# Kernel optimization log

Measured on AMD Instinct MI355X. Metric: run time of the kernel, lower is better.

Reference implementation:

```python
import jax, jax.numpy as jnp
import numpy as np

DIM = 768
NUM_HEADS = 12
HEAD_DIM = DIM // NUM_HEADS
H, W = 16, 64
HK, WK = 7, 11
N = H * W
B = 8
SCALE = HEAD_DIM ** -0.5


def build_local_mask():
    # Vectorized version of the original nested loop: for each token (h,w),
    # positions inside the hk x wk window are visible (0), others -inf.
    h_idx = np.repeat(np.arange(H), W)  # [N]
    w_idx = np.tile(np.arange(W), H)    # [N]
    hh = np.arange(H + HK - 1)
    ww = np.arange(W + WK - 1)
    in_h = (hh[None, :] >= h_idx[:, None]) & (hh[None, :] < h_idx[:, None] + HK)  # [N, H+hk-1]
    in_w = (ww[None, :] >= w_idx[:, None]) & (ww[None, :] < w_idx[:, None] + WK)  # [N, W+wk-1]
    visible = in_h[:, :, None] & in_w[:, None, :]  # [N, H+hk-1, W+wk-1]
    mask_big = np.where(visible, 0.0, 1.0).astype(np.float32)
    mask_crop = mask_big[:, HK // 2:H + HK // 2, WK // 2:W + WK // 2].reshape(N, N)
    mask = np.where(mask_crop < 1.0, mask_crop, np.float32(-np.inf))  # [N, N]
    return jnp.asarray(mask)[None, None]  # [1, 1, N, N]


def setup_inputs() -> dict:
    key = jax.random.key(0)
    k1, k2, k3 = jax.random.split(key, 3)
    x = jax.random.normal(k1, (B, N, DIM), dtype=jnp.float32)
    w_qkv = jax.random.normal(k2, (3 * DIM, DIM), dtype=jnp.float32) * 0.02  # torch Linear weight [out,in]
    w_proj = jax.random.normal(k3, (DIM, DIM), dtype=jnp.float32) * 0.02
    b_proj = jnp.zeros((DIM,), dtype=jnp.float32)
    mask = build_local_mask()
    return {"x": x, "w_qkv": w_qkv, "w_proj": w_proj, "b_proj": b_proj, "mask": mask}


def reference(x, w_qkv, w_proj, b_proj, mask):
    Bx, Nx, C = x.shape
    qkv = jnp.einsum('bnc,oc->bno', x, w_qkv)  # [B, N, 3*dim]
    qkv = qkv.reshape(Bx, Nx, 3, NUM_HEADS, HEAD_DIM).transpose(2, 0, 3, 1, 4)  # [3,B,h,N,d]
    q, k, v = qkv[0] * SCALE, qkv[1], qkv[2]
    attn = jnp.einsum('bhnd,bhmd->bhnm', q, k) + mask  # [B,h,N,N] with local -inf mask
    attn = jax.nn.softmax(attn, axis=-1)
    out = jnp.einsum('bhnm,bhmd->bhnd', attn, v)  # [B,h,N,d]
    out = out.transpose(0, 2, 1, 3).reshape(Bx, Nx, C)
    out = jnp.einsum('bnc,oc->bno', out, w_proj) + b_proj
    return out
```

## Files before the change

### kernel.cpp

```cpp
#include <hip/hip_runtime.h>
#include <hip/hip_bf16.h>
#include <stdint.h>

typedef __bf16 bf16;
typedef __bf16 bf16x8 __attribute__((ext_vector_type(8)));
typedef __bf16 bf16x4 __attribute__((ext_vector_type(4)));
typedef float f32x4 __attribute__((ext_vector_type(4)));

#define KDIM 768
#define NHEAD 12
#define HDIM 64
#define NTOK 1024
#define BATCH 8

#define SWZ(row, b) ((b) ^ (((row) & 7) << 4))

__device__ __forceinline__ void gl_lds16(const bf16* g, bf16* l) {
    __builtin_amdgcn_global_load_lds((const __attribute__((address_space(1))) void*)g,
                                     (__attribute__((address_space(3))) void*)l, 16, 0, 0);
}

__global__ void k_cvt_all(const float* __restrict__ x, const float* __restrict__ wq,
                          const float* __restrict__ wp, bf16* __restrict__ xb,
                          bf16* __restrict__ wqb, bf16* __restrict__ wpb) {
    int b = blockIdx.x;
    const float* src;
    bf16* dst;
    int base;
    if (b < 6144)       { src = x;  dst = xb;  base = b; }
    else if (b < 7872)  { src = wq; dst = wqb; base = b - 6144; }
    else                { src = wp; dst = wpb; base = b - 7872; }
    int i = (base * 256 + threadIdx.x) * 4;
    float4 v = *(const float4*)(src + i);
    bf16x4 o;
    o[0] = (bf16)v.x; o[1] = (bf16)v.y; o[2] = (bf16)v.z; o[3] = (bf16)v.w;
    *(bf16x4*)(dst + i) = o;
}

#define BM 128
#define BN 128
#define BK 32

#define STAGE_G(Ab, Wb, Abuf, Bbuf, k0) do {                                   \
    gl_lds16((Ab) + (size_t)sr0 * KDIM + (k0) + sc0, (Abuf) + wv * 512);        \
    gl_lds16((Ab) + (size_t)sr1 * KDIM + (k0) + sc1, (Abuf) + 2048 + wv * 512); \
    gl_lds16((Wb) + (size_t)sr0 * KDIM + (k0) + sc0, (Bbuf) + wv * 512);        \
    gl_lds16((Wb) + (size_t)sr1 * KDIM + (k0) + sc1, (Bbuf) + 2048 + wv * 512); \
} while (0)

#define GEMM_PRE()                                                              \
    const int t = threadIdx.x;                                                  \
    const int lane = t & 63;                                                    \
    const int wv = t >> 6;                                                      \
    const int wr = wv >> 1, wc = wv & 1;                                        \
    const int lr = lane & 15, lg = lane >> 4;                                   \
             \
    const int q0 = wv * 64 + lane;                                              \
    const int R0 = q0 >> 3, wp0 = (q0 & 7) ^ (R0 & 7);                          \
    const int sr0 = 2 * R0 + (wp0 >> 2), sc0 = (wp0 & 3) * 8;                   \
    const int q1 = 256 + wv * 64 + lane;                                        \
    const int R1 = q1 >> 3, wp1 = (q1 & 7) ^ (R1 & 7);                          \
    const int sr1 = 2 * R1 + (wp1 >> 2), sc1 = (wp1 & 3) * 8;                   \
                                                         \
    const int rhalf = lr >> 1;                                                  \
    const int xorp = (((lr & 1) * 64 + lg * 16) ^ (rhalf << 4));

#define GEMM_LOOP(Ab, Wb)                                                       \
    f32x4 acc[4][4] = {};                                                       \
    STAGE_G(Ab, Wb, As[0], Bs[0], 0);                                           \
    STAGE_G(Ab, Wb, As[1], Bs[1], BK);                                          \
    asm volatile("s_waitcnt vmcnt(4)" ::: "memory");                            \
    __builtin_amdgcn_s_barrier();                                               \
    for (int tt = 0; tt < 24; ++tt) {                                           \
        int p = tt & 1;                                                         \
        const char* Ab8 = (const char*)As[p];                                   \
        const char* Bb8 = (const char*)Bs[p];                                   \
        bf16x8 af[4], bfr[4];                                                   \
        _Pragma("unroll")                                                       \
        for (int m = 0; m < 4; ++m)                                             \
            af[m] = *(const bf16x8*)(Ab8 + (wr * 32 + m * 8 + rhalf) * 128 + xorp); \
        _Pragma("unroll")                                                       \
        for (int n = 0; n < 4; ++n)                                             \
            bfr[n] = *(const bf16x8*)(Bb8 + (wc * 32 + n * 8 + rhalf) * 128 + xorp); \
        asm volatile("s_waitcnt lgkmcnt(0)" ::: "memory");                      \
        __builtin_amdgcn_s_barrier();                                           \
        if (tt < 22) {                                                          \
            STAGE_G(Ab, Wb, As[p], Bs[p], (tt + 2) * BK);                       \
            __builtin_amdgcn_sched_barrier(0);                                  \
        }                                                                       \
        _Pragma("unroll")                                                       \
        for (int m = 0; m < 4; ++m)                                             \
            _Pragma("unroll")                                                   \
            for (int n = 0; n < 4; ++n)                                         \
                acc[m][n] = __builtin_amdgcn_mfma_f32_16x16x32_bf16(af[m], bfr[n], acc[m][n], 0, 0, 0); \
        if (tt < 22)       { asm volatile("s_waitcnt vmcnt(4)" ::: "memory"); } \
        else if (tt == 22) { asm volatile("s_waitcnt vmcnt(0)" ::: "memory"); } \
        __builtin_amdgcn_s_barrier();                                           \
    }

__global__ __launch_bounds__(256) void k_gemm_qkv(
    const bf16* __restrict__ A, const bf16* __restrict__ W,
    bf16* __restrict__ qb, bf16* __restrict__ kb, bf16* __restrict__ vb)
{
    __shared__ bf16 As[2][BM * BK];
    __shared__ bf16 Bs[2][BN * BK];
    GEMM_PRE();
    const int bm = blockIdx.x, bn = blockIdx.y;
    const bf16* Ab = A + (size_t)bm * BM * KDIM;
    const bf16* Wb = W + (size_t)bn * BN * KDIM;
    GEMM_LOOP(Ab, Wb);

    const float QSC = 0.18033688011112042f;
#pragma unroll
    for (int n = 0; n < 4; ++n) {
        int o = bn * BN + wc * 64 + n * 16 + lr;
        int s = o / 768;
        int rem = o - s * 768;
        int head = rem >> 6;
        int d = o & 63;
        bf16* dst = (s == 0) ? qb : ((s == 1) ? kb : vb);
        float sc = (s == 0) ? QSC : 1.0f;
#pragma unroll
        for (int m = 0; m < 4; ++m) {
            int grow = bm * BM + wr * 64 + m * 16 + lg * 4;
            int bidx = grow >> 10;
            int tok = grow & 1023;
            size_t base = (((size_t)bidx * NHEAD + head) * NTOK + tok) * HDIM + d;
#pragma unroll
            for (int r = 0; r < 4; ++r)
                dst[base + (size_t)r * HDIM] = (bf16)(acc[m][n][r] * sc);
        }
    }
}

__global__ __launch_bounds__(256) void k_gemm_proj(
    const bf16* __restrict__ A, const bf16* __restrict__ W,
    const float* __restrict__ bias, float* __restrict__ out)
{
    __shared__ bf16 As[2][BM * BK];
    __shared__ bf16 Bs[2][BN * BK];
    GEMM_PRE();
    const int bm = blockIdx.x, bn = blockIdx.y;
    const bf16* Ab = A + (size_t)bm * BM * KDIM;
    const bf16* Wb = W + (size_t)bn * BN * KDIM;
    GEMM_LOOP(Ab, Wb);

#pragma unroll
    for (int n = 0; n < 4; ++n) {
        int col = bn * BN + wc * 64 + n * 16 + lr;
        float bv = bias[col];
#pragma unroll
        for (int m = 0; m < 4; ++m) {
            int grow = bm * BM + wr * 64 + m * 16 + lg * 4;
#pragma unroll
            for (int r = 0; r < 4; ++r)
                out[(size_t)(grow + r) * KDIM + col] = acc[m][n][r] + bv;
        }
    }
}

__global__ __launch_bounds__(256) void k_attn(
    const bf16* __restrict__ qbuf, const bf16* __restrict__ kbuf,
    const bf16* __restrict__ vbuf, bf16* __restrict__ ob)
{
    const int x = blockIdx.x;
    const int sub = x >> 3;
    const int bh = (x & 7) * 12 + (sub >> 4);
    const int qblk = sub & 15;
    const int head = bh % NHEAD, bidx = bh / NHEAD;
    const bf16* Q  = qbuf + (size_t)bh * NTOK * HDIM;
    const bf16* Kp = kbuf + (size_t)bh * NTOK * HDIM;
    const bf16* Vp = vbuf + (size_t)bh * NTOK * HDIM;

    const int t = threadIdx.x, lane = t & 63, wv = t >> 6;
    const int lr = lane & 15, lg = lane >> 4, lkb = lg * 8;

    __shared__ bf16 Ks[2][64 * 64];
    __shared__ bf16 vT[2][64 * 64];
    __shared__ bf16 pls[4][16 * 64];

    {
        bf16x8 z = {};
        *(bf16x8*)&pls[wv][lane * 16] = z;
        *(bf16x8*)&pls[wv][lane * 16 + 8] = z;
    }

    bf16x8 qf[2];
#pragma unroll
    for (int ks = 0; ks < 2; ++ks)
        qf[ks] = *(const bf16x8*)(Q + (size_t)(qblk * 64 + wv * 16 + lr) * HDIM + ks * 32 + lkb);

    f32x4 acc[4] = {};
    float mrow[4] = {-1e30f, -1e30f, -1e30f, -1e30f};
    float lrow[4] = {0.f, 0.f, 0.f, 0.f};

    const int kh0 = (qblk - 3 < 0) ? 0 : qblk - 3;
    const int kh1 = (qblk + 3 > 15) ? 15 : qblk + 3;

    const int sj = t >> 2;
    const int sd = (t & 3) * 16;

    const bf16* ks0 = Kp + (size_t)(kh0 * 64 + sj) * HDIM + sd;
    const bf16* vs0 = Vp + (size_t)(kh0 * 64 + sj) * HDIM + sd;
    bf16x8 gk0 = *(const bf16x8*)ks0, gk1 = *(const bf16x8*)(ks0 + 8);
    bf16x8 gv0 = *(const bf16x8*)vs0, gv1 = *(const bf16x8*)(vs0 + 8);

    char* pb8 = (char*)pls[wv];
    const int wq0 = wv * 16 + lg * 4;
    int cur = 0;

    for (int kh = kh0; kh <= kh1; ++kh) {
        char* kb8 = (char*)Ks[cur];
        char* vb8 = (char*)vT[cur];
        {
            int kbo = sj * 128 + sd * 2;
            *(bf16x8*)(kb8 + SWZ(sj, kbo)) = gk0;
            *(bf16x8*)(kb8 + SWZ(sj, kbo + 16)) = gk1;
        }
#pragma unroll
        for (int ii = 0; ii < 8; ++ii) {
            int d = sd + ii;
            *(bf16*)(vb8 + SWZ(d, (d << 7) + (sj << 1))) = gv0[ii];
        }
#pragma unroll
        for (int ii = 0; ii < 8; ++ii) {
            int d = sd + 8 + ii;
            *(bf16*)(vb8 + SWZ(d, (d << 7) + (sj << 1))) = gv1[ii];
        }
        if (kh < kh1) {
            const bf16* kn = Kp + (size_t)((kh + 1) * 64 + sj) * HDIM + sd;
            const bf16* vn = Vp + (size_t)((kh + 1) * 64 + sj) * HDIM + sd;
            gk0 = *(const bf16x8*)kn; gk1 = *(const bf16x8*)(kn + 8);
            gv0 = *(const bf16x8*)vn; gv1 = *(const bf16x8*)(vn + 8);
        }
        asm volatile("s_waitcnt lgkmcnt(0)" ::: "memory");
        __builtin_amdgcn_s_barrier();

        f32x4 s[3];
#pragma unroll
        for (int jj = 0; jj < 3; ++jj) {
            int j = wv - 1 + jj;
            if (j >= 0 && j <= 3) {
                int key = j * 16 + lr;
                int kbase = key * 128;
                bf16x8 kf0 = *(const bf16x8*)(kb8 + SWZ(key, kbase + lg * 16));
                bf16x8 kf1 = *(const bf16x8*)(kb8 + SWZ(key, kbase + 64 + lg * 16));
                f32x4 sv = {};
                sv = __builtin_amdgcn_mfma_f32_16x16x32_bf16(qf[0], kf0, sv, 0, 0, 0);
                sv = __builtin_amdgcn_mfma_f32_16x16x32_bf16(qf[1], kf1, sv, 0, 0, 0);
#pragma unroll
                for (int r = 0; r < 4; ++r) {
                    int dw = wq0 + r - key;
                    sv[r] = (dw >= -5 && dw <= 5) ? sv[r] : -1e30f;
                }
                s[jj] = sv;
            } else {
                s[jj] = f32x4{-1e30f, -1e30f, -1e30f, -1e30f};
            }
        }

        float pm[4], scl[4];
#pragma unroll
        for (int r = 0; r < 4; ++r) pm[r] = fmaxf(fmaxf(s[0][r], s[1][r]), s[2][r]);
#pragma unroll
        for (int off = 1; off < 16; off <<= 1)
#pragma unroll
            for (int r = 0; r < 4; ++r) pm[r] = fmaxf(pm[r], __shfl_xor(pm[r], off));
#pragma unroll
        for (int r = 0; r < 4; ++r) {
            float mn = fmaxf(mrow[r], pm[r]);
            scl[r] = exp2f(mrow[r] - mn);
            mrow[r] = mn;
        }
#pragma unroll
        for (int dt = 0; dt < 4; ++dt)
#pragma unroll
            for (int r = 0; r < 4; ++r) acc[dt][r] *= scl[r];

        float psum[4] = {0.f, 0.f, 0.f, 0.f};
#pragma unroll
        for (int jj = 0; jj < 3; ++jj) {
            int j = wv - 1 + jj;
            if (j >= 0 && j <= 3) {
#pragma unroll
                for (int r = 0; r < 4; ++r) {
                    float p = exp2f(s[jj][r] - mrow[r]);
                    psum[r] += p;
                    int row = lg * 4 + r;
                    *(bf16*)(pb8 + SWZ(row, row * 128 + (j * 16 + lr) * 2)) = (bf16)p;
                }
            }
        }
#pragma unroll
        for (int r = 0; r < 4; ++r) lrow[r] = lrow[r] * scl[r] + psum[r];

        bf16x8 pf0 = *(const bf16x8*)(pb8 + SWZ(lr, lr * 128 + lg * 16));
        bf16x8 pf1 = *(const bf16x8*)(pb8 + SWZ(lr, lr * 128 + 64 + lg * 16));
#pragma unroll
        for (int dt = 0; dt < 4; ++dt) {
            int vrow = dt * 16 + lr;
            bf16x8 vf0 = *(const bf16x8*)(vb8 + SWZ(vrow, vrow * 128 + lg * 16));
            bf16x8 vf1 = *(const bf16x8*)(vb8 + SWZ(vrow, vrow * 128 + 64 + lg * 16));
            acc[dt] = __builtin_amdgcn_mfma_f32_16x16x32_bf16(pf0, vf0, acc[dt], 0, 0, 0);
            acc[dt] = __builtin_amdgcn_mfma_f32_16x16x32_bf16(pf1, vf1, acc[dt], 0, 0, 0);
        }
        cur ^= 1;
    }

#pragma unroll
    for (int off = 1; off < 16; off <<= 1)
#pragma unroll
        for (int r = 0; r < 4; ++r) lrow[r] += __shfl_xor(lrow[r], off);

#pragma unroll
    for (int r = 0; r < 4; ++r) {
        float inv = 1.0f / lrow[r];
        int tok = qblk * 64 + wv * 16 + lg * 4 + r;
        size_t rowbase = ((size_t)bidx * NTOK + tok) * KDIM + head * HDIM;
#pragma unroll
        for (int dt = 0; dt < 4; ++dt)
            ob[rowbase + dt * 16 + lr] = (bf16)(acc[dt][r] * inv);
    }
}

extern "C" void kernel_launch(void* const* d_in, const int* in_sizes, int n_in,
                              void* d_out, int out_size, void* d_ws, size_t ws_size,
                              hipStream_t stream) {
    const float* x      = (const float*)d_in[0];
    const float* w_qkv  = (const float*)d_in[1];
    const float* w_proj = (const float*)d_in[2];
    const float* b_proj = (const float*)d_in[3];
    float* out = (float*)d_out;

    char* ws = (char*)d_ws;
    bf16* xb  = (bf16*)(ws);
    bf16* wqb = (bf16*)(ws + 12582912);
    bf16* wpb = (bf16*)(ws + 16121856);
    bf16* qb  = (bf16*)(ws + 17301504);
    bf16* kb  = (bf16*)(ws + 29884416);
    bf16* vb  = (bf16*)(ws + 42467328);
    bf16* aob = (bf16*)(ws + 55050240);

    hipLaunchKernelGGL(k_cvt_all, dim3(8448), dim3(256), 0, stream, x, w_qkv, w_proj, xb, wqb, wpb);
    hipLaunchKernelGGL(k_gemm_qkv, dim3(64, 18), dim3(256), 0, stream, xb, wqb, qb, kb, vb);
    hipLaunchKernelGGL(k_attn,     dim3(1536), dim3(256), 0, stream, qb, kb, vb, aob);
    hipLaunchKernelGGL(k_gemm_proj, dim3(64, 6), dim3(256), 0, stream, aob, wpb, b_proj, out);
}
```

Baseline: 105.6 us.

## Rework GEMMs to 128x256 tiles with 8 waves and triple-buffered BK=64 pipeline

Replaces the 128x128, BK=32 double-buffered GEMM with a 128x256 tile computed by 512 threads (2x4 waves), a BK=64 K-step and a three-stage LDS ring. Global-to-LDS loads are split across two halves of each iteration and interleaved with MFMA groups, and setprio is raised around the MFMAs. The intent is more reuse per loaded byte, fewer barriers per FLOP and better overlap of loads with compute. In exchange it uses much more LDS (144 KB per block), which limits occupancy, and it launches fewer blocks (576 for QKV, 192 for the projection), which may underfill the GPU.

```diff
diff --git a/kernel.cpp b/kernel.cpp
--- a/kernel.cpp
+++ b/kernel.cpp
@@ -37,83 +37,120 @@
     *(bf16x4*)(dst + i) = o;
 }
 
-#define BM 128
-#define BN 128
-#define BK 32
-
-#define STAGE_G(Ab, Wb, Abuf, Bbuf, k0) do {                                   \
-    gl_lds16((Ab) + (size_t)sr0 * KDIM + (k0) + sc0, (Abuf) + wv * 512);        \
-    gl_lds16((Ab) + (size_t)sr1 * KDIM + (k0) + sc1, (Abuf) + 2048 + wv * 512); \
-    gl_lds16((Wb) + (size_t)sr0 * KDIM + (k0) + sc0, (Bbuf) + wv * 512);        \
-    gl_lds16((Wb) + (size_t)sr1 * KDIM + (k0) + sc1, (Bbuf) + 2048 + wv * 512); \
+
+#define G_MFMA(a, b, c) __builtin_amdgcn_mfma_f32_16x16x32_bf16(a, b, c, 0, 0, 0)
+
+#define LOADA(SC)                                                              \
+    _Pragma("unroll")                                                          \
+    for (int m = 0; m < 4; ++m) {                                              \
+        const char* rp = (const char*)sA[SC] + (wr * 64 + m * 16 + lr) * 128;  \
+        af[m][0] = *(const bf16x8*)(rp + k0off);                               \
+        af[m][1] = *(const bf16x8*)(rp + k1off);                               \
+    }
+
+#define LOADB(SC, n0, bfr)                                                     \
+    _Pragma("unroll")                                                          \
+    for (int nn = 0; nn < 2; ++nn) {                                           \
+        const char* rp = (const char*)sB[SC] + (wc * 64 + ((n0) + nn) * 16 + lr) * 128; \
+        bfr[nn][0] = *(const bf16x8*)(rp + k0off);                             \
+        bfr[nn][1] = *(const bf16x8*)(rp + k1off);                             \
+    }
+
+#define MMQ(ch, bfr)                                                           \
+    __builtin_amdgcn_s_setprio(1);                                             \
+    _Pragma("unroll")                                                          \
+    for (int m = 0; m < 4; ++m)                                                \
+        _Pragma("unroll")                                                      \
+        for (int nn = 0; nn < 2; ++nn) {                                       \
+            acc[m][2 * (ch) + nn] = G_MFMA(af[m][0], bfr[nn][0], acc[m][2 * (ch) + nn]); \
+            acc[m][2 * (ch) + nn] = G_MFMA(af[m][1], bfr[nn][1], acc[m][2 * (ch) + nn]); \
+        }                                                                      \
+    __builtin_amdgcn_s_setprio(0);
+
+#define ITER(SC, SS, kt) do {                                                  \
+    bf16x8 af[4][2];                                                           \
+    LOADA(SC);                                                                 \
+    bf16x8 b0[2][2];                                                           \
+    LOADB(SC, 0, b0);                                                          \
+    if ((kt) + 2 < NKT) {                                                      \
+        const bf16* As_ = Ab + (size_t)Rt * KDIM + ((kt) + 2) * 64 + wp8;      \
+        gl_lds16(As_,            &sA[SS][t * 8]);                              \
+        gl_lds16(As_ + 64 * KDIM, &sA[SS][t * 8 + 4096]);                      \
+        const bf16* Bs_ = Wb + (size_t)Rt * KDIM + ((kt) + 2) * 64 + wp8;      \
+        gl_lds16(Bs_,            &sB[SS][t * 8]);                              \
+        gl_lds16(Bs_ + 64 * KDIM, &sB[SS][t * 8 + 4096]);                      \
+    }                                                                          \
+    MMQ(0, b0);                                                                \
+    asm volatile("s_barrier" ::: "memory");                                    \
+    bf16x8 b1[2][2];                                                           \
+    LOADB(SC, 2, b1);                                                          \
+    if ((kt) + 2 < NKT) {                                                      \
+        const bf16* Bs_ = Wb + (size_t)Rt * KDIM + ((kt) + 2) * 64 + wp8;      \
+        gl_lds16(Bs_ + 128 * KDIM, &sB[SS][t * 8 + 8192]);                     \
+        gl_lds16(Bs_ + 192 * KDIM, &sB[SS][t * 8 + 12288]);                    \
+    }                                                                          \
+    MMQ(1, b1);                                                                \
+    if ((kt) <= NKT - 3)      { asm volatile("s_waitcnt vmcnt(6)" ::: "memory"); } \
+    else if ((kt) == NKT - 2) { asm volatile("s_waitcnt vmcnt(0)" ::: "memory"); } \
+    asm volatile("s_barrier" ::: "memory");                                    \
 } while (0)
 
-#define GEMM_PRE()                                                              \
-    const int t = threadIdx.x;                                                  \
-    const int lane = t & 63;                                                    \
-    const int wv = t >> 6;                                                      \
-    const int wr = wv >> 1, wc = wv & 1;                                        \
-    const int lr = lane & 15, lg = lane >> 4;                                   \
-             \
-    const int q0 = wv * 64 + lane;                                              \
-    const int R0 = q0 >> 3, wp0 = (q0 & 7) ^ (R0 & 7);                          \
-    const int sr0 = 2 * R0 + (wp0 >> 2), sc0 = (wp0 & 3) * 8;                   \
-    const int q1 = 256 + wv * 64 + lane;                                        \
-    const int R1 = q1 >> 3, wp1 = (q1 & 7) ^ (R1 & 7);                          \
-    const int sr1 = 2 * R1 + (wp1 >> 2), sc1 = (wp1 & 3) * 8;                   \
-                                                         \
-    const int rhalf = lr >> 1;                                                  \
-    const int xorp = (((lr & 1) * 64 + lg * 16) ^ (rhalf << 4));
-
-#define GEMM_LOOP(Ab, Wb)                                                       \
-    f32x4 acc[4][4] = {};                                                       \
-    STAGE_G(Ab, Wb, As[0], Bs[0], 0);                                           \
-    STAGE_G(Ab, Wb, As[1], Bs[1], BK);                                          \
-    asm volatile("s_waitcnt vmcnt(4)" ::: "memory");                            \
-    __builtin_amdgcn_s_barrier();                                               \
-    for (int tt = 0; tt < 24; ++tt) {                                           \
-        int p = tt & 1;                                                         \
-        const char* Ab8 = (const char*)As[p];                                   \
-        const char* Bb8 = (const char*)Bs[p];                                   \
-        bf16x8 af[4], bfr[4];                                                   \
-        _Pragma("unroll")                                                       \
-        for (int m = 0; m < 4; ++m)                                             \
-            af[m] = *(const bf16x8*)(Ab8 + (wr * 32 + m * 8 + rhalf) * 128 + xorp); \
-        _Pragma("unroll")                                                       \
-        for (int n = 0; n < 4; ++n)                                             \
-            bfr[n] = *(const bf16x8*)(Bb8 + (wc * 32 + n * 8 + rhalf) * 128 + xorp); \
-        asm volatile("s_waitcnt lgkmcnt(0)" ::: "memory");                      \
-        __builtin_amdgcn_s_barrier();                                           \
-        if (tt < 22) {                                                          \
-            STAGE_G(Ab, Wb, As[p], Bs[p], (tt + 2) * BK);                       \
-            __builtin_amdgcn_sched_barrier(0);                                  \
-        }                                                                       \
-        _Pragma("unroll")                                                       \
-        for (int m = 0; m < 4; ++m)                                             \
-            _Pragma("unroll")                                                   \
-            for (int n = 0; n < 4; ++n)                                         \
-                acc[m][n] = __builtin_amdgcn_mfma_f32_16x16x32_bf16(af[m], bfr[n], acc[m][n], 0, 0, 0); \
-        if (tt < 22)       { asm volatile("s_waitcnt vmcnt(4)" ::: "memory"); } \
-        else if (tt == 22) { asm volatile("s_waitcnt vmcnt(0)" ::: "memory"); } \
-        __builtin_amdgcn_s_barrier();                                           \
-    }
-
-__global__ __launch_bounds__(256) void k_gemm_qkv(
+#define NKT 12
+
+#define GEMM_BODY(A_PTR, W_PTR)                                                \
+    const int t = threadIdx.x;                                                 \
+    const int lane = t & 63;                                                   \
+    const int wv = t >> 6;                                           \
+    const int wr = wv >> 2, wc = wv & 3;                            \
+    const int lr = lane & 15, lg = lane >> 4;                                  \
+    const int xorb = (lr & 7) << 4;                                            \
+    const int k0off = (lg * 16) ^ xorb;                                        \
+    const int k1off = (64 + lg * 16) ^ xorb;                                   \
+    const int Rt = t >> 3;                               \
+    const int wp8 = ((t & 7) ^ (Rt & 7)) * 8;   \
+    const int bm = blockIdx.x, bn = blockIdx.y;                                \
+    const bf16* Ab = (A_PTR) + (size_t)bm * 128 * KDIM;                        \
+    const bf16* Wb = (W_PTR) + (size_t)bn * 256 * KDIM;                        \
+    f32x4 acc[4][4] = {};                                                      \
+                      \
+    {                                                                          \
+        const bf16* As_ = Ab + (size_t)Rt * KDIM + wp8;                        \
+        const bf16* Bs_ = Wb + (size_t)Rt * KDIM + wp8;                        \
+        gl_lds16(As_,             &sA[0][t * 8]);                              \
+        gl_lds16(As_ + 64 * KDIM, &sA[0][t * 8 + 4096]);                       \
+        gl_lds16(Bs_,             &sB[0][t * 8]);                              \
+        gl_lds16(Bs_ + 64 * KDIM, &sB[0][t * 8 + 4096]);                       \
+        gl_lds16(Bs_ + 128 * KDIM, &sB[0][t * 8 + 8192]);                      \
+        gl_lds16(Bs_ + 192 * KDIM, &sB[0][t * 8 + 12288]);                     \
+        gl_lds16(As_ + 64,             &sA[1][t * 8]);                         \
+        gl_lds16(As_ + 64 + 64 * KDIM, &sA[1][t * 8 + 4096]);                  \
+        gl_lds16(Bs_ + 64,             &sB[1][t * 8]);                         \
+        gl_lds16(Bs_ + 64 + 64 * KDIM, &sB[1][t * 8 + 4096]);                  \
+        gl_lds16(Bs_ + 64 + 128 * KDIM, &sB[1][t * 8 + 8192]);                 \
+        gl_lds16(Bs_ + 64 + 192 * KDIM, &sB[1][t * 8 + 12288]);                \
+    }                                                                          \
+    asm volatile("s_waitcnt vmcnt(6)" ::: "memory");                           \
+    asm volatile("s_barrier" ::: "memory");                                    \
+    _Pragma("unroll 1")                                                        \
+    for (int g = 0; g < 4; ++g) {                                              \
+        int kt = g * 3;                                                        \
+        ITER(0, 2, kt);                                                        \
+        ITER(1, 0, kt + 1);                                                    \
+        ITER(2, 1, kt + 2);                                                    \
+    }
+
+__global__ __launch_bounds__(512) void k_gemm_qkv(
     const bf16* __restrict__ A, const bf16* __restrict__ W,
     bf16* __restrict__ qb, bf16* __restrict__ kb, bf16* __restrict__ vb)
 {
-    __shared__ bf16 As[2][BM * BK];
-    __shared__ bf16 Bs[2][BN * BK];
-    GEMM_PRE();
-    const int bm = blockIdx.x, bn = blockIdx.y;
-    const bf16* Ab = A + (size_t)bm * BM * KDIM;
-    const bf16* Wb = W + (size_t)bn * BN * KDIM;
-    GEMM_LOOP(Ab, Wb);
+    __shared__ __attribute__((aligned(16))) bf16 sA[3][8192];
+    __shared__ __attribute__((aligned(16))) bf16 sB[3][16384];
+    GEMM_BODY(A, W);
 
     const float QSC = 0.18033688011112042f;
 #pragma unroll
     for (int n = 0; n < 4; ++n) {
-        int o = bn * BN + wc * 64 + n * 16 + lr;
+        int o = bn * 256 + wc * 64 + n * 16 + lr;
         int s = o / 768;
         int rem = o - s * 768;
         int head = rem >> 6;
@@ -122,7 +159,7 @@
         float sc = (s == 0) ? QSC : 1.0f;
 #pragma unroll
         for (int m = 0; m < 4; ++m) {
-            int grow = bm * BM + wr * 64 + m * 16 + lg * 4;
+            int grow = bm * 128 + wr * 64 + m * 16 + lg * 4;
             int bidx = grow >> 10;
             int tok = grow & 1023;
             size_t base = (((size_t)bidx * NHEAD + head) * NTOK + tok) * HDIM + d;
@@ -133,25 +170,21 @@
     }
 }
 
-__global__ __launch_bounds__(256) void k_gemm_proj(
+__global__ __launch_bounds__(512) void k_gemm_proj(
     const bf16* __restrict__ A, const bf16* __restrict__ W,
     const float* __restrict__ bias, float* __restrict__ out)
 {
-    __shared__ bf16 As[2][BM * BK];
-    __shared__ bf16 Bs[2][BN * BK];
-    GEMM_PRE();
-    const int bm = blockIdx.x, bn = blockIdx.y;
-    const bf16* Ab = A + (size_t)bm * BM * KDIM;
-    const bf16* Wb = W + (size_t)bn * BN * KDIM;
-    GEMM_LOOP(Ab, Wb);
+    __shared__ __attribute__((aligned(16))) bf16 sA[3][8192];
+    __shared__ __attribute__((aligned(16))) bf16 sB[3][16384];
+    GEMM_BODY(A, W);
 
 #pragma unroll
     for (int n = 0; n < 4; ++n) {
-        int col = bn * BN + wc * 64 + n * 16 + lr;
+        int col = bn * 256 + wc * 64 + n * 16 + lr;
         float bv = bias[col];
 #pragma unroll
         for (int m = 0; m < 4; ++m) {
-            int grow = bm * BM + wr * 64 + m * 16 + lg * 4;
+            int grow = bm * 128 + wr * 64 + m * 16 + lg * 4;
 #pragma unroll
             for (int r = 0; r < 4; ++r)
                 out[(size_t)(grow + r) * KDIM + col] = acc[m][n][r] + bv;
@@ -342,7 +375,7 @@
     bf16* aob = (bf16*)(ws + 55050240);
 
     hipLaunchKernelGGL(k_cvt_all, dim3(8448), dim3(256), 0, stream, x, w_qkv, w_proj, xb, wqb, wpb);
-    hipLaunchKernelGGL(k_gemm_qkv, dim3(64, 18), dim3(256), 0, stream, xb, wqb, qb, kb, vb);
+    hipLaunchKernelGGL(k_gemm_qkv, dim3(64, 9), dim3(512), 0, stream, xb, wqb, qb, kb, vb);
     hipLaunchKernelGGL(k_attn,     dim3(1536), dim3(256), 0, stream, qb, kb, vb, aob);
-    hipLaunchKernelGGL(k_gemm_proj, dim3(64, 6), dim3(256), 0, stream, aob, wpb, b_proj, out);
-}
+    hipLaunchKernelGGL(k_gemm_proj, dim3(64, 3), dim3(512), 0, stream, aob, wpb, b_proj, out);
+}
```

Measured after the change: 116.7 us. 10.5% more time.

## Restructure GEMMs to 128x192 tiles with triple-buffered LDS and interleaved loads

Applied to the files above, without the earlier changes.

Both GEMM kernels move from a 128x128 double-buffered tile to a 128x192 tile with a three-stage LDS ring. Global-to-LDS loads for two tiles ahead are split between two MFMA halves, with s_setprio raised around the MFMAs and only one barrier per K step. A new swizzle matches the 64-byte row layout. The aim is better overlap of memory and MFMA work, more reuse per block and fewer barriers. The cost is fewer blocks (768 and 256), which may leave CUs idle on a 256-CU part.

```diff
diff --git a/kernel.cpp b/kernel.cpp
--- a/kernel.cpp
+++ b/kernel.cpp
@@ -37,83 +37,99 @@
     *(bf16x4*)(dst + i) = o;
 }
 
-#define BM 128
-#define BN 128
-#define BK 32
-
-#define STAGE_G(Ab, Wb, Abuf, Bbuf, k0) do {                                   \
-    gl_lds16((Ab) + (size_t)sr0 * KDIM + (k0) + sc0, (Abuf) + wv * 512);        \
-    gl_lds16((Ab) + (size_t)sr1 * KDIM + (k0) + sc1, (Abuf) + 2048 + wv * 512); \
-    gl_lds16((Wb) + (size_t)sr0 * KDIM + (k0) + sc0, (Bbuf) + wv * 512);        \
-    gl_lds16((Wb) + (size_t)sr1 * KDIM + (k0) + sc1, (Bbuf) + 2048 + wv * 512); \
+
+#define G_MFMA(a, b, c) __builtin_amdgcn_mfma_f32_16x16x32_bf16(a, b, c, 0, 0, 0)
+#define NT3 24
+
+#define TILE_ITER(SC, SS, kt) do {                                               \
+    const char* Ab8 = (const char*)sA[SC];                                       \
+    const char* Bb8 = (const char*)sB[SC];                                       \
+    bf16x8 af[4];                                                                \
+    _Pragma("unroll")                                                            \
+    for (int m = 0; m < 4; ++m)                                                  \
+        af[m] = *(const bf16x8*)(Ab8 + (wr * 64 + m * 16 + lr) * 64 + kxoff);    \
+    bf16x8 bfr[3];                                                               \
+    _Pragma("unroll")                                                            \
+    for (int n = 0; n < 3; ++n)                                                  \
+        bfr[n] = *(const bf16x8*)(Bb8 + (wc * 96 + n * 16 + lr) * 64 + kxoff);   \
+    if ((kt) < NT3 - 2) {                                                        \
+        int k2 = ((kt) + 2) * 32;                                                \
+        gl_lds16(Ab + (size_t)srow * KDIM + k2 + spos,        &sA[SS][t * 8]);         \
+        gl_lds16(Ab + (size_t)(64 + srow) * KDIM + k2 + spos, &sA[SS][t * 8 + 2048]);  \
+        gl_lds16(Wb + (size_t)srow * KDIM + k2 + spos,        &sB[SS][t * 8]);         \
+    }                                                                            \
+    __builtin_amdgcn_s_setprio(1);                                               \
+    _Pragma("unroll")                                                            \
+    for (int m = 0; m < 4; ++m)                                                  \
+        _Pragma("unroll")                                                        \
+        for (int n = 0; n < 3; ++n)                                              \
+            acc[m][n] = G_MFMA(af[m], bfr[n], acc[m][n]);                        \
+    __builtin_amdgcn_s_setprio(0);                                               \
+    _Pragma("unroll")                                                            \
+    for (int n = 0; n < 3; ++n)                                                  \
+        bfr[n] = *(const bf16x8*)(Bb8 + (wc * 96 + (n + 3) * 16 + lr) * 64 + kxoff); \
+    if ((kt) < NT3 - 2) {                                                        \
+        int k2 = ((kt) + 2) * 32;                                                \
+        gl_lds16(Wb + (size_t)(64 + srow) * KDIM + k2 + spos,  &sB[SS][t * 8 + 2048]); \
+        gl_lds16(Wb + (size_t)(128 + srow) * KDIM + k2 + spos, &sB[SS][t * 8 + 4096]); \
+    }                                                                            \
+    __builtin_amdgcn_s_setprio(1);                                               \
+    _Pragma("unroll")                                                            \
+    for (int m = 0; m < 4; ++m)                                                  \
+        _Pragma("unroll")                                                        \
+        for (int n = 0; n < 3; ++n)                                              \
+            acc[m][n + 3] = G_MFMA(af[m], bfr[n], acc[m][n + 3]);                \
+    __builtin_amdgcn_s_setprio(0);                                               \
+    if ((kt) < NT3 - 2)       { asm volatile("s_waitcnt vmcnt(5)" ::: "memory"); } \
+    else if ((kt) == NT3 - 2) { asm volatile("s_waitcnt vmcnt(0)" ::: "memory"); } \
+    asm volatile("s_barrier" ::: "memory");                                      \
 } while (0)
 
-#define GEMM_PRE()                                                              \
-    const int t = threadIdx.x;                                                  \
-    const int lane = t & 63;                                                    \
-    const int wv = t >> 6;                                                      \
-    const int wr = wv >> 1, wc = wv & 1;                                        \
-    const int lr = lane & 15, lg = lane >> 4;                                   \
-             \
-    const int q0 = wv * 64 + lane;                                              \
-    const int R0 = q0 >> 3, wp0 = (q0 & 7) ^ (R0 & 7);                          \
-    const int sr0 = 2 * R0 + (wp0 >> 2), sc0 = (wp0 & 3) * 8;                   \
-    const int q1 = 256 + wv * 64 + lane;                                        \
-    const int R1 = q1 >> 3, wp1 = (q1 & 7) ^ (R1 & 7);                          \
-    const int sr1 = 2 * R1 + (wp1 >> 2), sc1 = (wp1 & 3) * 8;                   \
-                                                         \
-    const int rhalf = lr >> 1;                                                  \
-    const int xorp = (((lr & 1) * 64 + lg * 16) ^ (rhalf << 4));
-
-#define GEMM_LOOP(Ab, Wb)                                                       \
-    f32x4 acc[4][4] = {};                                                       \
-    STAGE_G(Ab, Wb, As[0], Bs[0], 0);                                           \
-    STAGE_G(Ab, Wb, As[1], Bs[1], BK);                                          \
-    asm volatile("s_waitcnt vmcnt(4)" ::: "memory");                            \
-    __builtin_amdgcn_s_barrier();                                               \
-    for (int tt = 0; tt < 24; ++tt) {                                           \
-        int p = tt & 1;                                                         \
-        const char* Ab8 = (const char*)As[p];                                   \
-        const char* Bb8 = (const char*)Bs[p];                                   \
-        bf16x8 af[4], bfr[4];                                                   \
-        _Pragma("unroll")                                                       \
-        for (int m = 0; m < 4; ++m)                                             \
-            af[m] = *(const bf16x8*)(Ab8 + (wr * 32 + m * 8 + rhalf) * 128 + xorp); \
-        _Pragma("unroll")                                                       \
-        for (int n = 0; n < 4; ++n)                                             \
-            bfr[n] = *(const bf16x8*)(Bb8 + (wc * 32 + n * 8 + rhalf) * 128 + xorp); \
-        asm volatile("s_waitcnt lgkmcnt(0)" ::: "memory");                      \
-        __builtin_amdgcn_s_barrier();                                           \
-        if (tt < 22) {                                                          \
-            STAGE_G(Ab, Wb, As[p], Bs[p], (tt + 2) * BK);                       \
-            __builtin_amdgcn_sched_barrier(0);                                  \
-        }                                                                       \
-        _Pragma("unroll")                                                       \
-        for (int m = 0; m < 4; ++m)                                             \
-            _Pragma("unroll")                                                   \
-            for (int n = 0; n < 4; ++n)                                         \
-                acc[m][n] = __builtin_amdgcn_mfma_f32_16x16x32_bf16(af[m], bfr[n], acc[m][n], 0, 0, 0); \
-        if (tt < 22)       { asm volatile("s_waitcnt vmcnt(4)" ::: "memory"); } \
-        else if (tt == 22) { asm volatile("s_waitcnt vmcnt(0)" ::: "memory"); } \
-        __builtin_amdgcn_s_barrier();                                           \
-    }
-
-__global__ __launch_bounds__(256) void k_gemm_qkv(
+#define GEMM_BODY(A_PTR, W_PTR)                                                  \
+    const int t = threadIdx.x;                                                   \
+    const int lane = t & 63;                                                     \
+    const int wv = t >> 6;                                             \
+    const int wr = wv >> 1, wc = wv & 1;                    \
+    const int lr = lane & 15, lg = lane >> 4;                                    \
+    const int kxoff = (lg << 4) ^ (((lr >> 1) & 3) << 4);                        \
+    const int srow = t >> 2;                               \
+    const int spos = (((t & 3) ^ ((t >> 3) & 3))) * 8;     \
+    const int bm = blockIdx.x, bn = blockIdx.y;                                  \
+    const bf16* Ab = (A_PTR) + (size_t)bm * 128 * KDIM;                          \
+    const bf16* Wb = (W_PTR) + (size_t)bn * 192 * KDIM;                          \
+    f32x4 acc[4][6] = {};                                                        \
+                                   \
+    gl_lds16(Ab + (size_t)srow * KDIM + spos,              &sA[0][t * 8]);       \
+    gl_lds16(Ab + (size_t)(64 + srow) * KDIM + spos,       &sA[0][t * 8 + 2048]);\
+    gl_lds16(Wb + (size_t)srow * KDIM + spos,              &sB[0][t * 8]);       \
+    gl_lds16(Wb + (size_t)(64 + srow) * KDIM + spos,       &sB[0][t * 8 + 2048]);\
+    gl_lds16(Wb + (size_t)(128 + srow) * KDIM + spos,      &sB[0][t * 8 + 4096]);\
+    gl_lds16(Ab + (size_t)srow * KDIM + 32 + spos,         &sA[1][t * 8]);       \
+    gl_lds16(Ab + (size_t)(64 + srow) * KDIM + 32 + spos,  &sA[1][t * 8 + 2048]);\
+    gl_lds16(Wb + (size_t)srow * KDIM + 32 + spos,         &sB[1][t * 8]);       \
+    gl_lds16(Wb + (size_t)(64 + srow) * KDIM + 32 + spos,  &sB[1][t * 8 + 2048]);\
+    gl_lds16(Wb + (size_t)(128 + srow) * KDIM + 32 + spos, &sB[1][t * 8 + 4096]);\
+    asm volatile("s_waitcnt vmcnt(5)" ::: "memory");                             \
+    asm volatile("s_barrier" ::: "memory");                                      \
+    _Pragma("unroll 1")                                                          \
+    for (int g = 0; g < 8; ++g) {                                                \
+        TILE_ITER(0, 2, g * 3);                                                  \
+        TILE_ITER(1, 0, g * 3 + 1);                                              \
+        TILE_ITER(2, 1, g * 3 + 2);                                              \
+    }
+
+__global__ __launch_bounds__(256, 2) void k_gemm_qkv(
     const bf16* __restrict__ A, const bf16* __restrict__ W,
     bf16* __restrict__ qb, bf16* __restrict__ kb, bf16* __restrict__ vb)
 {
-    __shared__ bf16 As[2][BM * BK];
-    __shared__ bf16 Bs[2][BN * BK];
-    GEMM_PRE();
-    const int bm = blockIdx.x, bn = blockIdx.y;
-    const bf16* Ab = A + (size_t)bm * BM * KDIM;
-    const bf16* Wb = W + (size_t)bn * BN * KDIM;
-    GEMM_LOOP(Ab, Wb);
+    __shared__ __attribute__((aligned(16))) bf16 sA[3][4096];
+    __shared__ __attribute__((aligned(16))) bf16 sB[3][6144];
+    GEMM_BODY(A, W);
 
     const float QSC = 0.18033688011112042f;
 #pragma unroll
-    for (int n = 0; n < 4; ++n) {
-        int o = bn * BN + wc * 64 + n * 16 + lr;
+    for (int n = 0; n < 6; ++n) {
+        int o = bn * 192 + wc * 96 + n * 16 + lr;
         int s = o / 768;
         int rem = o - s * 768;
         int head = rem >> 6;
@@ -122,7 +138,7 @@
         float sc = (s == 0) ? QSC : 1.0f;
 #pragma unroll
         for (int m = 0; m < 4; ++m) {
-            int grow = bm * BM + wr * 64 + m * 16 + lg * 4;
+            int grow = bm * 128 + wr * 64 + m * 16 + lg * 4;
             int bidx = grow >> 10;
             int tok = grow & 1023;
             size_t base = (((size_t)bidx * NHEAD + head) * NTOK + tok) * HDIM + d;
@@ -133,25 +149,21 @@
     }
 }
 
-__global__ __launch_bounds__(256) void k_gemm_proj(
+__global__ __launch_bounds__(256, 2) void k_gemm_proj(
     const bf16* __restrict__ A, const bf16* __restrict__ W,
     const float* __restrict__ bias, float* __restrict__ out)
 {
-    __shared__ bf16 As[2][BM * BK];
-    __shared__ bf16 Bs[2][BN * BK];
-    GEMM_PRE();
-    const int bm = blockIdx.x, bn = blockIdx.y;
-    const bf16* Ab = A + (size_t)bm * BM * KDIM;
-    const bf16* Wb = W + (size_t)bn * BN * KDIM;
-    GEMM_LOOP(Ab, Wb);
-
-#pragma unroll
-    for (int n = 0; n < 4; ++n) {
-        int col = bn * BN + wc * 64 + n * 16 + lr;
+    __shared__ __attribute__((aligned(16))) bf16 sA[3][4096];
+    __shared__ __attribute__((aligned(16))) bf16 sB[3][6144];
+    GEMM_BODY(A, W);
+
+#pragma unroll
+    for (int n = 0; n < 6; ++n) {
+        int col = bn * 192 + wc * 96 + n * 16 + lr;
         float bv = bias[col];
 #pragma unroll
         for (int m = 0; m < 4; ++m) {
-            int grow = bm * BM + wr * 64 + m * 16 + lg * 4;
+            int grow = bm * 128 + wr * 64 + m * 16 + lg * 4;
 #pragma unroll
             for (int r = 0; r < 4; ++r)
                 out[(size_t)(grow + r) * KDIM + col] = acc[m][n][r] + bv;
@@ -342,7 +354,7 @@
     bf16* aob = (bf16*)(ws + 55050240);
 
     hipLaunchKernelGGL(k_cvt_all, dim3(8448), dim3(256), 0, stream, x, w_qkv, w_proj, xb, wqb, wpb);
-    hipLaunchKernelGGL(k_gemm_qkv, dim3(64, 18), dim3(256), 0, stream, xb, wqb, qb, kb, vb);
+    hipLaunchKernelGGL(k_gemm_qkv, dim3(64, 12), dim3(256), 0, stream, xb, wqb, qb, kb, vb);
     hipLaunchKernelGGL(k_attn,     dim3(1536), dim3(256), 0, stream, qb, kb, vb, aob);
-    hipLaunchKernelGGL(k_gemm_proj, dim3(64, 6), dim3(256), 0, stream, aob, wpb, b_proj, out);
-}
+    hipLaunchKernelGGL(k_gemm_proj, dim3(64, 4), dim3(256), 0, stream, aob, wpb, b_proj, out);
+}
```

Result: slower. 111.5 us (+5.6%).

## Restructure GEMMs: A operands direct to registers, 128x192 tiles, triple-buffered B

Applied to the files above, without the earlier changes.

Both GEMM kernels are rewritten so each wave loads its A fragments straight from global memory into registers, prefetched two k-steps ahead. Only the weight tile goes through LDS, now triple-buffered with three-tile-deep async prefetch. The output tile grows from 128x128 to 128x192, so grids shrink to 64x12 and 64x4 and each block reuses more of its loads. MFMA sections raise wave priority, and launch bounds request two blocks per CU. The trade-offs are more register pressure, fewer blocks in flight, and uncoalesced 16-byte row loads for A.

```diff
diff --git a/kernel.cpp b/kernel.cpp
--- a/kernel.cpp
+++ b/kernel.cpp
@@ -37,83 +37,93 @@
     *(bf16x4*)(dst + i) = o;
 }
 
-#define BM 128
-#define BN 128
-#define BK 32
-
-#define STAGE_G(Ab, Wb, Abuf, Bbuf, k0) do {                                   \
-    gl_lds16((Ab) + (size_t)sr0 * KDIM + (k0) + sc0, (Abuf) + wv * 512);        \
-    gl_lds16((Ab) + (size_t)sr1 * KDIM + (k0) + sc1, (Abuf) + 2048 + wv * 512); \
-    gl_lds16((Wb) + (size_t)sr0 * KDIM + (k0) + sc0, (Bbuf) + wv * 512);        \
-    gl_lds16((Wb) + (size_t)sr1 * KDIM + (k0) + sc1, (Bbuf) + 2048 + wv * 512); \
+
+#define G_MFMA(a, b, c) __builtin_amdgcn_mfma_f32_16x16x32_bf16(a, b, c, 0, 0, 0)
+#define NT 24
+#define VMW(N) asm volatile("s_waitcnt vmcnt(" #N ")" ::: "memory")
+
+#define LD_A(P, kt) do {                                                        \
+    P[0] = *(const bf16x8*)(Arow + (size_t)(kt) * 32);                          \
+    P[1] = *(const bf16x8*)(Arow + 12288 + (size_t)(kt) * 32);                  \
+    P[2] = *(const bf16x8*)(Arow + 24576 + (size_t)(kt) * 32);                  \
+    P[3] = *(const bf16x8*)(Arow + 36864 + (size_t)(kt) * 32);                  \
 } while (0)
 
-#define GEMM_PRE()                                                              \
+#define ST_B(wsp, kt) do {                                                      \
+    const bf16* Bs_ = Wst + (size_t)(kt) * 32;                                  \
+    gl_lds16(Bs_,             (wsp) + t * 8);                                   \
+    gl_lds16(Bs_ + 64 * 768,  (wsp) + t * 8 + 2048);                            \
+    gl_lds16(Bs_ + 128 * 768, (wsp) + t * 8 + 4096);                            \
+} while (0)
+
+#define TILE(PCUR, PNXT, rsp, wsp, kt) do {                                     \
+    if ((kt) + 2 < NT) LD_A(PNXT, (kt) + 2);                                    \
+    if ((kt) + 3 < NT) ST_B(wsp, (kt) + 3);                                     \
+    bf16x8 bfr[6];                                                              \
+    _Pragma("unroll")                                                           \
+    for (int n = 0; n < 6; ++n)                                                 \
+        bfr[n] = *(const bf16x8*)((const char*)(rsp) + (wc * 96 + n * 16 + lr) * 64 + kxoff); \
+    __builtin_amdgcn_s_setprio(1);                                              \
+    _Pragma("unroll")                                                           \
+    for (int m = 0; m < 4; ++m)                                                 \
+        _Pragma("unroll")                                                       \
+        for (int n = 0; n < 6; ++n)                                             \
+            acc[m][n] = G_MFMA(PCUR[m], bfr[n], acc[m][n]);                     \
+    __builtin_amdgcn_s_setprio(0);                                              \
+} while (0)
+
+#define GEMM_BODY(A_PTR, W_PTR)                                                 \
     const int t = threadIdx.x;                                                  \
     const int lane = t & 63;                                                    \
     const int wv = t >> 6;                                                      \
     const int wr = wv >> 1, wc = wv & 1;                                        \
     const int lr = lane & 15, lg = lane >> 4;                                   \
-             \
-    const int q0 = wv * 64 + lane;                                              \
-    const int R0 = q0 >> 3, wp0 = (q0 & 7) ^ (R0 & 7);                          \
-    const int sr0 = 2 * R0 + (wp0 >> 2), sc0 = (wp0 & 3) * 8;                   \
-    const int q1 = 256 + wv * 64 + lane;                                        \
-    const int R1 = q1 >> 3, wp1 = (q1 & 7) ^ (R1 & 7);                          \
-    const int sr1 = 2 * R1 + (wp1 >> 2), sc1 = (wp1 & 3) * 8;                   \
-                                                         \
-    const int rhalf = lr >> 1;                                                  \
-    const int xorp = (((lr & 1) * 64 + lg * 16) ^ (rhalf << 4));
-
-#define GEMM_LOOP(Ab, Wb)                                                       \
-    f32x4 acc[4][4] = {};                                                       \
-    STAGE_G(Ab, Wb, As[0], Bs[0], 0);                                           \
-    STAGE_G(Ab, Wb, As[1], Bs[1], BK);                                          \
-    asm volatile("s_waitcnt vmcnt(4)" ::: "memory");                            \
+    const int kxoff = (lg << 4) ^ (((lr >> 1) & 3) << 4);                       \
+    const int srow = t >> 2;                                                    \
+    const int spos = (((t & 3) ^ ((t >> 3) & 3))) * 8;                          \
+    const int bm = blockIdx.x, bn = blockIdx.y;                                 \
+    const bf16* Ab = (A_PTR) + (size_t)bm * 128 * KDIM;                         \
+    const bf16* Wb = (W_PTR) + (size_t)bn * 192 * KDIM;                         \
+    const bf16* Arow = Ab + (size_t)(wr * 64 + lr) * KDIM + lg * 8;             \
+    const bf16* Wst  = Wb + (size_t)srow * KDIM + spos;                         \
+    f32x4 acc[4][6] = {};                                                       \
+    bf16x8 pA[4], pB[4], pC[4];                                                 \
+    LD_A(pA, 0);                                                                \
+    LD_A(pB, 1);                                                                \
+    ST_B(&sB[0][0], 0);                                                         \
+    ST_B(&sB[1][0], 1);                                                         \
+    ST_B(&sB[2][0], 2);                                                         \
+    VMW(6);                                                                     \
     __builtin_amdgcn_s_barrier();                                               \
-    for (int tt = 0; tt < 24; ++tt) {                                           \
-        int p = tt & 1;                                                         \
-        const char* Ab8 = (const char*)As[p];                                   \
-        const char* Bb8 = (const char*)Bs[p];                                   \
-        bf16x8 af[4], bfr[4];                                                   \
-        _Pragma("unroll")                                                       \
-        for (int m = 0; m < 4; ++m)                                             \
-            af[m] = *(const bf16x8*)(Ab8 + (wr * 32 + m * 8 + rhalf) * 128 + xorp); \
-        _Pragma("unroll")                                                       \
-        for (int n = 0; n < 4; ++n)                                             \
-            bfr[n] = *(const bf16x8*)(Bb8 + (wc * 32 + n * 8 + rhalf) * 128 + xorp); \
-        asm volatile("s_waitcnt lgkmcnt(0)" ::: "memory");                      \
+    _Pragma("unroll 1")                                                         \
+    for (int g = 0; g < 8; ++g) {                                               \
+        int kt = g * 3;                                                         \
+        bf16* rs = &sB[(g & 1) * 3][0];                                         \
+        bf16* ws = &sB[((g & 1) ^ 1) * 3][0];                                   \
+        TILE(pA, pC, rs, ws, kt);                                               \
+        if (g < 7) { VMW(14); } else { VMW(11); }                               \
         __builtin_amdgcn_s_barrier();                                           \
-        if (tt < 22) {                                                          \
-            STAGE_G(Ab, Wb, As[p], Bs[p], (tt + 2) * BK);                       \
-            __builtin_amdgcn_sched_barrier(0);                                  \
+        TILE(pB, pA, rs + 6144, ws + 6144, kt + 1);                             \
+        if (g < 7) { VMW(14); } else { VMW(4); }                                \
+        __builtin_amdgcn_s_barrier();                                           \
+        TILE(pC, pB, rs + 12288, ws + 12288, kt + 2);                           \
+        if (g < 7) {                                                            \
+            VMW(14);                                                            \
+            __builtin_amdgcn_s_barrier();                                       \
         }                                                                       \
-        _Pragma("unroll")                                                       \
-        for (int m = 0; m < 4; ++m)                                             \
-            _Pragma("unroll")                                                   \
-            for (int n = 0; n < 4; ++n)                                         \
-                acc[m][n] = __builtin_amdgcn_mfma_f32_16x16x32_bf16(af[m], bfr[n], acc[m][n], 0, 0, 0); \
-        if (tt < 22)       { asm volatile("s_waitcnt vmcnt(4)" ::: "memory"); } \
-        else if (tt == 22) { asm volatile("s_waitcnt vmcnt(0)" ::: "memory"); } \
-        __builtin_amdgcn_s_barrier();                                           \
-    }
-
-__global__ __launch_bounds__(256) void k_gemm_qkv(
+    }
+
+__global__ __launch_bounds__(256, 2) void k_gemm_qkv(
     const bf16* __restrict__ A, const bf16* __restrict__ W,
     bf16* __restrict__ qb, bf16* __restrict__ kb, bf16* __restrict__ vb)
 {
-    __shared__ bf16 As[2][BM * BK];
-    __shared__ bf16 Bs[2][BN * BK];
-    GEMM_PRE();
-    const int bm = blockIdx.x, bn = blockIdx.y;
-    const bf16* Ab = A + (size_t)bm * BM * KDIM;
-    const bf16* Wb = W + (size_t)bn * BN * KDIM;
-    GEMM_LOOP(Ab, Wb);
+    __shared__ __attribute__((aligned(16))) bf16 sB[6][6144];
+    GEMM_BODY(A, W);
 
     const float QSC = 0.18033688011112042f;
 #pragma unroll
-    for (int n = 0; n < 4; ++n) {
-        int o = bn * BN + wc * 64 + n * 16 + lr;
+    for (int n = 0; n < 6; ++n) {
+        int o = bn * 192 + wc * 96 + n * 16 + lr;
         int s = o / 768;
         int rem = o - s * 768;
         int head = rem >> 6;
@@ -122,7 +132,7 @@
         float sc = (s == 0) ? QSC : 1.0f;
 #pragma unroll
         for (int m = 0; m < 4; ++m) {
-            int grow = bm * BM + wr * 64 + m * 16 + lg * 4;
+            int grow = bm * 128 + wr * 64 + m * 16 + lg * 4;
             int bidx = grow >> 10;
             int tok = grow & 1023;
             size_t base = (((size_t)bidx * NHEAD + head) * NTOK + tok) * HDIM + d;
@@ -133,25 +143,20 @@
     }
 }
 
-__global__ __launch_bounds__(256) void k_gemm_proj(
+__global__ __launch_bounds__(256, 2) void k_gemm_proj(
     const bf16* __restrict__ A, const bf16* __restrict__ W,
     const float* __restrict__ bias, float* __restrict__ out)
 {
-    __shared__ bf16 As[2][BM * BK];
-    __shared__ bf16 Bs[2][BN * BK];
-    GEMM_PRE();
-    const int bm = blockIdx.x, bn = blockIdx.y;
-    const bf16* Ab = A + (size_t)bm * BM * KDIM;
-    const bf16* Wb = W + (size_t)bn * BN * KDIM;
-    GEMM_LOOP(Ab, Wb);
-
-#pragma unroll
-    for (int n = 0; n < 4; ++n) {
-        int col = bn * BN + wc * 64 + n * 16 + lr;
+    __shared__ __attribute__((aligned(16))) bf16 sB[6][6144];
+    GEMM_BODY(A, W);
+
+#pragma unroll
+    for (int n = 0; n < 6; ++n) {
+        int col = bn * 192 + wc * 96 + n * 16 + lr;
         float bv = bias[col];
 #pragma unroll
         for (int m = 0; m < 4; ++m) {
-            int grow = bm * BM + wr * 64 + m * 16 + lg * 4;
+            int grow = bm * 128 + wr * 64 + m * 16 + lg * 4;
 #pragma unroll
             for (int r = 0; r < 4; ++r)
                 out[(size_t)(grow + r) * KDIM + col] = acc[m][n][r] + bv;
@@ -342,7 +347,7 @@
     bf16* aob = (bf16*)(ws + 55050240);
 
     hipLaunchKernelGGL(k_cvt_all, dim3(8448), dim3(256), 0, stream, x, w_qkv, w_proj, xb, wqb, wpb);
-    hipLaunchKernelGGL(k_gemm_qkv, dim3(64, 18), dim3(256), 0, stream, xb, wqb, qb, kb, vb);
+    hipLaunchKernelGGL(k_gemm_qkv, dim3(64, 12), dim3(256), 0, stream, xb, wqb, qb, kb, vb);
     hipLaunchKernelGGL(k_attn,     dim3(1536), dim3(256), 0, stream, qb, kb, vb, aob);
-    hipLaunchKernelGGL(k_gemm_proj, dim3(64, 6), dim3(256), 0, stream, aob, wpb, b_proj, out);
-}
+    hipLaunchKernelGGL(k_gemm_proj, dim3(64, 4), dim3(256), 0, stream, aob, wpb, b_proj, out);
+}
```

Measured after the change: 126.1 us. 19.4% more time.
